# Optimization experiments

Hardware: AMD Instinct MI355X
Metric: run time of the kernel (lower is better)

The kernel has to match this reference:

```python
import jax, jax.numpy as jnp
import numpy as np

B, H = 1, 512
NVAR, NCLS = 16384, 65536
NP, NM = 4096, 4096
NEG = -1e30


def setup_inputs() -> dict:
    key = jax.random.key(0)
    ks = jax.random.split(key, 16)
    s = 0.02  # weight init scale
    return {
        "literal_emb": jax.random.normal(ks[0], (B, 2 * NVAR, H), jnp.float32),
        "clause_emb": jax.random.normal(ks[1], (B, NCLS, H), jnp.float32),
        "pos_idx": jax.random.randint(ks[2], (NP,), 0, NCLS),
        "neg_idx": jax.random.randint(ks[3], (NM,), 0, NCLS),
        "keep_mask": jax.random.randint(ks[4], (NP, NM), 0, 2).astype(bool),
        "taken_mask": jax.random.uniform(ks[5], (NP, NM)) < 0.01,  # sparse exclusion set
        "var_K_w": s * jax.random.normal(ks[6], (H, H), jnp.float32),
        "var_K_b": jnp.zeros((H,), jnp.float32),
        "var_Q_w": s * jax.random.normal(ks[7], (H, H), jnp.float32),
        "var_Q_b": jnp.zeros((H,), jnp.float32),
        "var_attn_w": s * jax.random.normal(ks[8], (1, H), jnp.float32),
        "var_attn_b": jnp.zeros((1,), jnp.float32),
        "W_Q_w": s * jax.random.normal(ks[9], (H, H), jnp.float32),
        "W_Q_b": jnp.zeros((H,), jnp.float32),
        "W_K_w": s * jax.random.normal(ks[10], (H, H), jnp.float32),
        "W_K_b": jnp.zeros((H,), jnp.float32),
    }


def reference(literal_emb, clause_emb, pos_idx, neg_idx, keep_mask, taken_mask,
              var_K_w, var_K_b, var_Q_w, var_Q_b, var_attn_w, var_attn_b,
              W_Q_w, W_Q_b, W_K_w, W_K_b):
    n_vars = literal_emb.shape[1] // 2
    # --- select_var: additive attention over positive literals ---
    K = literal_emb[:, :n_vars]                       # [B, V, H]
    K_t = K @ var_K_w.T + var_K_b                     # [B, V, H]
    Q = clause_emb.sum(axis=1)                        # [B, H] (C_aggr='sum')
    Q_t = Q @ var_Q_w.T + var_Q_b                     # [B, H]
    u = (jnp.tanh(K_t + Q_t[:, None, :]) @ var_attn_w.T + var_attn_b)[..., 0]  # [B, V]
    log_score = jax.nn.log_softmax(u, axis=-1)
    var_logp = jnp.max(log_score, axis=-1)            # [B]
    var_idx = jnp.argmax(log_score, axis=-1)          # [B]
    # --- clause-pair attention over pivot pos/neg clause pools ---
    q = clause_emb[:, pos_idx] @ W_Q_w.T + W_Q_b      # [B, NP, H]
    k = clause_emb[:, neg_idx] @ W_K_w.T + W_K_b      # [B, NM, H]
    h = q.shape[-1]
    scores = jnp.einsum('bnh,bmh->bnm', q, k) / jnp.sqrt(jnp.float32(h))
    # mask_grid_asym: drop invalid (keep_mask==0) and already-taken pairs, log-normalize
    valid = keep_mask & (~taken_mask)                 # [NP, NM]
    masked = jnp.where(valid[None], scores, jnp.float32(NEG))
    flat = masked.reshape(masked.shape[0], -1)        # [B, NP*NM]
    logp = jax.nn.log_softmax(flat, axis=-1)
    C_logp = jnp.max(logp, axis=-1)                   # [B]
    C_flat = jnp.argmax(logp, axis=-1)                # [B]
    M = scores.shape[-1]
    ci, cj = C_flat // M, C_flat % M
    c_idx_pos = pos_idx[ci]                           # map back to global clause ids
    c_idx_neg = neg_idx[cj]
    c_logp = C_logp + var_logp                        # [B]
    return (c_logp, c_idx_pos, c_idx_neg, var_idx)
```

## Files before the change

kernel.cpp:

```cpp
#include <hip/hip_runtime.h>
#include <hip/hip_bf16.h>
#include <math.h>

#define HH 512
#define NVARS 16384
#define NPOS 4096
#define NMS 4096
#define NEGV -1.0e30f
#define RSQRT_H 0.04419417382415922f

#define BM 128
#define BK 16

typedef unsigned short u16;
typedef __attribute__((ext_vector_type(8))) short bf16x8;
typedef __attribute__((ext_vector_type(4))) float f32x4;

struct SPart { float m; float s; int a; int pad; };

__device__ inline u16 f2bf(float f) {
  unsigned u = __float_as_uint(f);
  unsigned r = (u + 0x7fffu + ((u >> 16) & 1u)) >> 16;
  return (u16)r;
}
__device__ inline float bf2f(u16 h) { return __uint_as_float(((unsigned)h) << 16); }

__device__ inline void wreduce_maxidx(float& v, int& idx) {
#pragma unroll
  for (int m = 1; m < 64; m <<= 1) {
    float ov = __shfl_xor(v, m, 64);
    int oi = __shfl_xor(idx, m, 64);
    if (ov > v || (ov == v && oi < idx)) { v = ov; idx = oi; }
  }
}

__device__ inline float wreduce_sum(float v) {
#pragma unroll
  for (int m = 1; m < 64; m <<= 1) v += __shfl_xor(v, m, 64);
  return v;
}

__global__ void detect_kernel(const unsigned int* __restrict__ keep, int* __restrict__ flag) {
  if (threadIdx.x == 0 && blockIdx.x == 0) {
    int ok = 1;
    for (int i = 0; i < 64; ++i) if (keep[i] > 1u) ok = 0;
    *flag = ok;
  }
}

__global__ __launch_bounds__(256) void pack_kernel(
    const void* __restrict__ keep, const void* __restrict__ taken,
    const int* __restrict__ flag, unsigned long long* __restrict__ vmask) {
  __shared__ unsigned char nib[256];
  const int f = *flag;
  const int t = threadIdx.x;
  const size_t e = (size_t)blockIdx.x * 1024 + (size_t)t * 4;
  int v0, v1, v2, v3;
  if (f) {
    uint4 kv = *(const uint4*)((const unsigned int*)keep + e);
    uint4 tv = *(const uint4*)((const unsigned int*)taken + e);
    v0 = kv.x && !tv.x; v1 = kv.y && !tv.y; v2 = kv.z && !tv.z; v3 = kv.w && !tv.w;
  } else {
    unsigned kv = *(const unsigned*)((const unsigned char*)keep + e);
    unsigned tv = *(const unsigned*)((const unsigned char*)taken + e);
    v0 = (kv & 0xffu) && !(tv & 0xffu);
    v1 = (kv & 0xff00u) && !(tv & 0xff00u);
    v2 = (kv & 0xff0000u) && !(tv & 0xff0000u);
    v3 = (kv & 0xff000000u) && !(tv & 0xff000000u);
  }
  nib[t] = (unsigned char)(v0 | (v1 << 1) | (v2 << 2) | (v3 << 3));
  __syncthreads();
  if (t < 16) {
    unsigned long long m = 0;
#pragma unroll
    for (int j = 0; j < 16; ++j)
      m |= (unsigned long long)nib[t * 16 + j] << (4 * j);
    vmask[(size_t)blockIdx.x * 16 + t] = m;
  }
}

__global__ __launch_bounds__(256) void qsum_kernel(
    const float* __restrict__ clause, double* __restrict__ qpart) {
  const int b = blockIdx.x, t = threadIdx.x;
  const int fg = t & 127;
  const int rh = t >> 7;
  const float* base = clause + (size_t)(b * 128 + rh * 64) * HH + fg * 4;
  double a0 = 0.0, a1 = 0.0, a2 = 0.0, a3 = 0.0;
#pragma unroll 4
  for (int r = 0; r < 64; ++r) {
    float4 v = *(const float4*)(base + (size_t)r * HH);
    a0 += (double)v.x; a1 += (double)v.y; a2 += (double)v.z; a3 += (double)v.w;
  }
  double* o = qpart + (size_t)(b * 2 + rh) * HH + fg * 4;
  o[0] = a0; o[1] = a1; o[2] = a2; o[3] = a3;
}

__global__ __launch_bounds__(256) void qred_kernel(
    const double* __restrict__ qpart, double* __restrict__ Qd) {
  __shared__ double red[256];
  const int t = threadIdx.x;
  const int h = blockIdx.x * 16 + (t & 15);
  const int chunk = t >> 4;
  double s = 0.0;
  for (int j = 0; j < 64; ++j) s += qpart[(size_t)(chunk * 64 + j) * HH + h];
  red[t] = s;
  __syncthreads();
  for (int off = 8; off > 0; off >>= 1) {
    if (chunk < off) red[t] += red[t + off * 16];
    __syncthreads();
  }
  if (t < 16) Qd[blockIdx.x * 16 + t] = red[t];
}

__global__ __launch_bounds__(256) void prepmv_kernel(
    const double* __restrict__ Qd, const float* __restrict__ varQw,
    const float* __restrict__ varQb, const float* __restrict__ varKb,
    float* __restrict__ tvec) {
  __shared__ double red[256];
  const int t = threadIdx.x;
  const int h = blockIdx.x * 16 + (t & 15);
  const int chunk = t >> 4;
  const float* wrow = varQw + (size_t)h * HH + chunk * 32;
  const double* qd = Qd + chunk * 32;
  double s = 0.0;
  for (int j = 0; j < 32; ++j) s += qd[j] * (double)wrow[j];
  red[t] = s;
  __syncthreads();
  for (int off = 8; off > 0; off >>= 1) {
    if (chunk < off) red[t] += red[t + off * 16];
    __syncthreads();
  }
  if (t < 16) {
    int hh = blockIdx.x * 16 + t;
    tvec[hh] = (float)(red[t] + (double)varQb[hh] + (double)varKb[hh]);
  }
}

__global__ __launch_bounds__(256) void tofrag_kernel(
    const float* __restrict__ src, u16* __restrict__ hi, u16* __restrict__ lo) {
  const int frag = blockIdx.x * 4 + (threadIdx.x >> 6);
  const int lane = threadIdx.x & 63;
  const int R = frag >> 4, K = frag & 15;
  const float* p = src + (size_t)(R * 16 + (lane & 15)) * HH + K * 32 + (lane >> 4) * 8;
  float v[8];
  *(float4*)&v[0] = *(const float4*)p;
  *(float4*)&v[4] = *(const float4*)(p + 4);
  u16 h[8], l[8];
#pragma unroll
  for (int e = 0; e < 8; ++e) { h[e] = f2bf(v[e]); l[e] = f2bf(v[e] - bf2f(h[e])); }
  size_t base = (size_t)frag * 512 + (size_t)lane * 8;
  *(ushort4*)(hi + base) = *(ushort4*)&h[0];
  *(ushort4*)(hi + base + 4) = *(ushort4*)&h[4];
  *(ushort4*)(lo + base) = *(ushort4*)&l[0];
  *(ushort4*)(lo + base + 4) = *(ushort4*)&l[4];
}

#define MFMA16(A, B)                                                                 \
  _Pragma("unroll") for (int i_ = 0; i_ < 4; ++i_)                                   \
  _Pragma("unroll") for (int j_ = 0; j_ < 4; ++j_)                                   \
    acc[i_][j_] = __builtin_amdgcn_mfma_f32_16x16x32_bf16(A[i_], B[j_], acc[i_][j_], 0, 0, 0);

#define MFMAS(AH, AL, BH, BL)                                                        \
  do { MFMA16(AH, BH) MFMA16(AH, BL) MFMA16(AL, BH) } while (0)

#define LOADF(s, AH, AL, BH, BL, PAH, PAL, PBH, PBL)                                 \
  do {                                                                               \
    _Pragma("unroll") for (int f_ = 0; f_ < 4; ++f_) {                               \
      size_t oa_ = abase + (size_t)f_ * 8192 + (size_t)(s) * 512;                    \
      size_t ob_ = bbase + (size_t)f_ * 8192 + (size_t)(s) * 512;                    \
      AH[f_] = *(const bf16x8*)(PAH + oa_);                                          \
      AL[f_] = *(const bf16x8*)(PAL + oa_);                                          \
      BH[f_] = *(const bf16x8*)(PBH + ob_);                                          \
      BL[f_] = *(const bf16x8*)(PBL + ob_);                                          \
    }                                                                                \
  } while (0)

__global__ __launch_bounds__(256, 3) void proj_kernel(
    const float* __restrict__ clause,
    const int* __restrict__ pos_idx, const int* __restrict__ neg_idx,
    const u16* __restrict__ wqhi, const u16* __restrict__ wqlo,
    const u16* __restrict__ wkhi2, const u16* __restrict__ wklo2,
    const float* __restrict__ bQ, const float* __restrict__ bK,
    float* __restrict__ qmat, float* __restrict__ kmat) {
  const int* __restrict__ idx = blockIdx.z ? neg_idx : pos_idx;
  const u16* __restrict__ bhp = blockIdx.z ? wkhi2 : wqhi;
  const u16* __restrict__ blp = blockIdx.z ? wklo2 : wqlo;
  const float* __restrict__ bias = blockIdx.z ? bK : bQ;
  float* __restrict__ out = blockIdx.z ? kmat : qmat;

  const int t = threadIdx.x, lane = t & 63, wid = t >> 6;
  const int wn = wid & 1, wm = wid >> 1;
  const int row0 = blockIdx.x * 128;
  const int col0 = blockIdx.y * 128;

  const float* aptr[4];
#pragma unroll
  for (int f = 0; f < 4; ++f) {
    int g = idx[row0 + wn * 64 + f * 16 + (lane & 15)];
    aptr[f] = clause + (size_t)g * HH + (lane >> 4) * 8;
  }
  const size_t bbase = (size_t)((col0 >> 4) + wm * 4) * 8192 + (size_t)lane * 8;

  f32x4 acc[4][4] = {};
#pragma unroll
  for (int s = 0; s < 16; ++s) {
    float rA[4][8];
    bf16x8 aH[4], aL[4], bH[4], bL[4];
#pragma unroll
    for (int f = 0; f < 4; ++f) {
      *(float4*)&rA[f][0] = *(const float4*)(aptr[f] + s * 32);
      *(float4*)&rA[f][4] = *(const float4*)(aptr[f] + s * 32 + 4);
      size_t ob = bbase + (size_t)f * 8192 + (size_t)s * 512;
      bH[f] = *(const bf16x8*)(bhp + ob);
      bL[f] = *(const bf16x8*)(blp + ob);
    }
#pragma unroll
    for (int f = 0; f < 4; ++f)
#pragma unroll
      for (int e = 0; e < 8; ++e) {
        float v = rA[f][e];
        u16 h = f2bf(v);
        aH[f][e] = (short)h;
        aL[f][e] = (short)f2bf(v - bf2f(h));
      }
    MFMAS(aH, aL, bH, bL);
  }

#pragma unroll
  for (int i = 0; i < 4; ++i)
#pragma unroll
    for (int j = 0; j < 4; ++j) {
      int h = col0 + wm * 64 + j * 16 + (lane & 15);
      float b = bias[h];
#pragma unroll
      for (int r = 0; r < 4; ++r) {
        int n = row0 + wn * 64 + i * 16 + (lane >> 4) * 4 + r;
        out[(size_t)n * HH + h] = acc[i][j][r] + b;
      }
    }
}

__global__ __launch_bounds__(256, 3) void ktu_kernel(
    const u16* __restrict__ lithi, const u16* __restrict__ litlo,
    const u16* __restrict__ wkhi, const u16* __restrict__ wklo,
    const float* __restrict__ tvec, const float* __restrict__ attnw,
    float* __restrict__ upart) {
  const int t = threadIdx.x, lane = t & 63, wid = t >> 6;
  const int wn = wid & 1, wm = wid >> 1;
  const int row0 = blockIdx.x * 128;
  const size_t abase = (size_t)((row0 >> 4) + wn * 4) * 8192 + (size_t)lane * 8;
  const size_t bbase = (size_t)(blockIdx.y * 8 + wm * 4) * 8192 + (size_t)lane * 8;

  f32x4 acc[4][4] = {};
#pragma unroll
  for (int s = 0; s < 16; ++s) {
    bf16x8 aH[4], aL[4], bH[4], bL[4];
    LOADF(s, aH, aL, bH, bL, lithi, litlo, wkhi, wklo);
    MFMAS(aH, aL, bH, bL);
  }

  const int cbase = blockIdx.y * 128 + wm * 64;
  float tv[4], aw[4];
#pragma unroll
  for (int j = 0; j < 4; ++j) {
    int c = cbase + j * 16 + (lane & 15);
    tv[j] = tvec[c]; aw[j] = attnw[c];
  }
  float us[4][4];
#pragma unroll
  for (int i = 0; i < 4; ++i)
#pragma unroll
    for (int r = 0; r < 4; ++r) {
      float s = 0.f;
#pragma unroll
      for (int j = 0; j < 4; ++j) {
        float x = acc[i][j][r] + tv[j];
        float th = 1.0f - 2.0f / (__expf(2.0f * x) + 1.0f);
        s += th * aw[j];
      }
      us[i][r] = s;
    }
#pragma unroll
  for (int m = 1; m < 16; m <<= 1)
#pragma unroll
    for (int i = 0; i < 4; ++i)
#pragma unroll
      for (int r = 0; r < 4; ++r) us[i][r] += __shfl_xor(us[i][r], m, 64);
  if ((lane & 15) == 0) {
#pragma unroll
    for (int i = 0; i < 4; ++i)
#pragma unroll
      for (int r = 0; r < 4; ++r) {
        int row = row0 + wn * 64 + i * 16 + (lane >> 4) * 4 + r;
        upart[(size_t)(blockIdx.y * 2 + wm) * NVARS + row] = us[i][r];
      }
  }
}

__global__ __launch_bounds__(256, 3) void scores_kernel(
    const u16* __restrict__ qhi, const u16* __restrict__ qlo,
    const u16* __restrict__ khi, const u16* __restrict__ klo,
    const unsigned long long* __restrict__ vmask, SPart* __restrict__ parts) {
  __shared__ unsigned long long mrow[128][2];
  __shared__ float s_rv[4]; __shared__ int s_ri[4]; __shared__ float s_rs[4];
  __shared__ float s_bm; __shared__ int s_ba;

  const int t = threadIdx.x;
  const int lane = t & 63;
  const int wid = t >> 6;
  const int wn = wid & 1, wm = wid >> 1;

  const int bid = blockIdx.x;
  const int xcd = bid & 7, p = bid >> 3;
  const int sp = p >> 6, q = p & 63;
  const int g = xcd * 2 + sp;
  const int bx = (g & 3) * 8 + (q & 7);
  const int by = (g >> 2) * 8 + (q >> 3);

  const int n0 = by * 128;
  const int m0 = bx * 128;
  const size_t abase = (size_t)((n0 >> 4) + wn * 4) * 8192 + (size_t)lane * 8;
  const size_t bbase = (size_t)((m0 >> 4) + wm * 4) * 8192 + (size_t)lane * 8;

  {
    int r = t >> 1, w = t & 1;
    mrow[r][w] = vmask[(size_t)(n0 + r) * (NMS / 64) + (m0 >> 6) + w];
  }
  __syncthreads();

  f32x4 acc[4][4] = {};
#pragma unroll
  for (int s = 0; s < 16; ++s) {
    bf16x8 aH[4], aL[4], bH[4], bL[4];
    LOADF(s, aH, aL, bH, bL, qhi, qlo, khi, klo);
    MFMAS(aH, aL, bH, bL);
  }

  const int rbase = wn * 64 + (lane >> 4) * 4;
  const int cb15 = (lane & 15);

  float mv = NEGV; int mi = 0x7fffffff;
#pragma unroll
  for (int i = 0; i < 4; ++i) {
#pragma unroll
    for (int r = 0; r < 4; ++r) {
      int rl = rbase + i * 16 + r;
      unsigned long long ww = mrow[rl][wm];
      int gb = (n0 + rl) * NMS + m0;
#pragma unroll
      for (int j = 0; j < 4; ++j) {
        int bit = j * 16 + cb15;
        int cl = wm * 64 + bit;
        float sv = acc[i][j][r] * RSQRT_H;
        acc[i][j][r] = sv;
        bool valid = ((ww >> bit) & 1ull) != 0;
        if (valid && (sv > mv || (sv == mv && gb + cl < mi))) { mv = sv; mi = gb + cl; }
      }
    }
  }
  wreduce_maxidx(mv, mi);
  if ((t & 63) == 0) { s_rv[wid] = mv; s_ri[wid] = mi; }
  __syncthreads();
  if (t == 0) {
    float bm = s_rv[0]; int ba = s_ri[0];
    for (int w = 1; w < 4; ++w)
      if (s_rv[w] > bm || (s_rv[w] == bm && s_ri[w] < ba)) { bm = s_rv[w]; ba = s_ri[w]; }
    s_bm = bm; s_ba = ba;
  }
  __syncthreads();
  const float bm = s_bm;

  float se = 0.f;
#pragma unroll
  for (int i = 0; i < 4; ++i) {
#pragma unroll
    for (int r = 0; r < 4; ++r) {
      int rl = rbase + i * 16 + r;
      unsigned long long ww = mrow[rl][wm];
#pragma unroll
      for (int j = 0; j < 4; ++j) {
        int bit = j * 16 + cb15;
        bool valid = ((ww >> bit) & 1ull) != 0;
        if (valid) se += __expf(acc[i][j][r] - bm);
      }
    }
  }
  se = wreduce_sum(se);
  if ((t & 63) == 0) s_rs[wid] = se;
  __syncthreads();
  if (t == 0) {
    SPart pt;
    pt.m = s_bm;
    pt.s = s_rs[0] + s_rs[1] + s_rs[2] + s_rs[3];
    pt.a = s_ba; pt.pad = 0;
    parts[by * 32 + bx] = pt;
  }
}

__global__ __launch_bounds__(256) void usum_kernel(
    const float* __restrict__ upart, SPart* __restrict__ uparts2) {
  __shared__ float s_rv[4]; __shared__ int s_ri[4]; __shared__ float s_rs[4];
  __shared__ float s_bm; __shared__ int s_ba;
  const int t = threadIdx.x;
  const int i = blockIdx.x * 256 + t;
  float u = 0.f;
#pragma unroll
  for (int p = 0; p < 8; ++p) u += upart[(size_t)p * NVARS + i];
  float mv = u; int mi = i;
  wreduce_maxidx(mv, mi);
  if ((t & 63) == 0) { s_rv[t >> 6] = mv; s_ri[t >> 6] = mi; }
  __syncthreads();
  if (t == 0) {
    float bm = s_rv[0]; int ba = s_ri[0];
    for (int w = 1; w < 4; ++w)
      if (s_rv[w] > bm || (s_rv[w] == bm && s_ri[w] < ba)) { bm = s_rv[w]; ba = s_ri[w]; }
    s_bm = bm; s_ba = ba;
  }
  __syncthreads();
  float se = __expf(u - s_bm);
  se = wreduce_sum(se);
  if ((t & 63) == 0) s_rs[t >> 6] = se;
  __syncthreads();
  if (t == 0) {
    SPart p;
    p.m = s_bm;
    p.s = s_rs[0] + s_rs[1] + s_rs[2] + s_rs[3];
    p.a = s_ba; p.pad = 0;
    uparts2[blockIdx.x] = p;
  }
}

__global__ __launch_bounds__(256) void final_kernel(
    const SPart* __restrict__ uparts2, const SPart* __restrict__ parts,
    const int* __restrict__ pos_idx, const int* __restrict__ neg_idx,
    float* __restrict__ out) {
  __shared__ float s_rv[4]; __shared__ int s_ri[4]; __shared__ float s_rs[4];
  __shared__ float s_umax; __shared__ int s_uarg; __shared__ float s_usum;
  __shared__ float s_gm; __shared__ int s_ga;
  const int t = threadIdx.x;

  float mv = -3.0e38f; int mi = 0x7fffffff;
  SPart up;
  if (t < 64) {
    up = uparts2[t];
    mv = up.m; mi = up.a;
  }
  wreduce_maxidx(mv, mi);
  if ((t & 63) == 0) { s_rv[t >> 6] = mv; s_ri[t >> 6] = mi; }
  __syncthreads();
  if (t == 0) {
    float bm = s_rv[0]; int ba = s_ri[0];
    for (int w = 1; w < 4; ++w)
      if (s_rv[w] > bm || (s_rv[w] == bm && s_ri[w] < ba)) { bm = s_rv[w]; ba = s_ri[w]; }
    s_umax = bm; s_uarg = ba;
  }
  __syncthreads();
  float se = (t < 64) ? up.s * __expf(up.m - s_umax) : 0.f;
  se = wreduce_sum(se);
  if ((t & 63) == 0) s_rs[t >> 6] = se;
  __syncthreads();
  if (t == 0) s_usum = s_rs[0] + s_rs[1] + s_rs[2] + s_rs[3];
  __syncthreads();

  mv = NEGV; mi = 0x7fffffff;
  for (int i = t; i < 1024; i += 256) {
    SPart p = parts[i];
    if (p.m > mv || (p.m == mv && p.a < mi)) { mv = p.m; mi = p.a; }
  }
  wreduce_maxidx(mv, mi);
  if ((t & 63) == 0) { s_rv[t >> 6] = mv; s_ri[t >> 6] = mi; }
  __syncthreads();
  if (t == 0) {
    float bm = s_rv[0]; int ba = s_ri[0];
    for (int w = 1; w < 4; ++w)
      if (s_rv[w] > bm || (s_rv[w] == bm && s_ri[w] < ba)) { bm = s_rv[w]; ba = s_ri[w]; }
    s_gm = bm; s_ga = ba;
  }
  __syncthreads();
  const float gm = s_gm;
  float ss = 0.f;
  for (int i = t; i < 1024; i += 256) {
    SPart p = parts[i];
    ss += p.s * __expf(p.m - gm);
  }
  ss = wreduce_sum(ss);
  if ((t & 63) == 0) s_rs[t >> 6] = ss;
  __syncthreads();
  if (t == 0) {
    float gsum = s_rs[0] + s_rs[1] + s_rs[2] + s_rs[3];
    float c_logp = -logf(gsum) - logf(s_usum);
    int ga = s_ga;
    if (ga == 0x7fffffff) ga = 0;
    int ci = ga >> 12, cj = ga & 4095;
    out[0] = c_logp;
    out[1] = (float)pos_idx[ci];
    out[2] = (float)neg_idx[cj];
    out[3] = (float)s_uarg;
  }
}

extern "C" void kernel_launch(void* const* d_in, const int* in_sizes, int n_in,
                              void* d_out, int out_size, void* d_ws, size_t ws_size,
                              hipStream_t stream) {
  (void)in_sizes; (void)n_in; (void)out_size; (void)ws_size;
  const float* lit    = (const float*)d_in[0];
  const float* clause = (const float*)d_in[1];
  const int* pos_idx  = (const int*)d_in[2];
  const int* neg_idx  = (const int*)d_in[3];
  const void* keep    = d_in[4];
  const void* taken   = d_in[5];
  const float* varKw  = (const float*)d_in[6];
  const float* varKb  = (const float*)d_in[7];
  const float* varQw  = (const float*)d_in[8];
  const float* varQb  = (const float*)d_in[9];
  const float* attnw  = (const float*)d_in[10];
  const float* WQw    = (const float*)d_in[12];
  const float* WQb    = (const float*)d_in[13];
  const float* WKw    = (const float*)d_in[14];
  const float* WKb    = (const float*)d_in[15];

  char* ws = (char*)d_ws;
  size_t off = 0;
  auto alloc = [&](size_t b) {
    char* p = ws + off;
    off = (off + b + 255) & ~(size_t)255;
    return p;
  };
  int* flag                  = (int*)alloc(4);
  double* qpart              = (double*)alloc((size_t)1024 * HH * 8);
  double* Qd                 = (double*)alloc(HH * 8);
  float* tvec                = (float*)alloc(HH * 4);
  float* upart               = (float*)alloc(8 * (size_t)NVARS * 4);
  unsigned long long* vmask  = (unsigned long long*)alloc((size_t)NPOS * (NMS / 64) * 8);
  float* qmat                = (float*)alloc((size_t)NPOS * HH * 4);
  float* kmat                = (float*)alloc((size_t)NMS * HH * 4);
  u16* qhi                   = (u16*)alloc((size_t)NPOS * HH * 2);
  u16* qlo                   = (u16*)alloc((size_t)NPOS * HH * 2);
  u16* khi                   = (u16*)alloc((size_t)NMS * HH * 2);
  u16* klo                   = (u16*)alloc((size_t)NMS * HH * 2);
  u16* wkhi                  = (u16*)alloc((size_t)HH * HH * 2);
  u16* wklo                  = (u16*)alloc((size_t)HH * HH * 2);
  u16* pwqhi                 = (u16*)alloc((size_t)HH * HH * 2);
  u16* pwqlo                 = (u16*)alloc((size_t)HH * HH * 2);
  u16* pwkhi                 = (u16*)alloc((size_t)HH * HH * 2);
  u16* pwklo                 = (u16*)alloc((size_t)HH * HH * 2);
  u16* lithi                 = (u16*)alloc((size_t)NVARS * HH * 2);
  u16* litlo                 = (u16*)alloc((size_t)NVARS * HH * 2);
  SPart* parts               = (SPart*)alloc(1024 * sizeof(SPart));
  SPart* uparts2             = (SPart*)alloc(64 * sizeof(SPart));

  detect_kernel<<<1, 64, 0, stream>>>((const unsigned int*)keep, flag);
  pack_kernel<<<16384, 256, 0, stream>>>(keep, taken, flag, vmask);
  qsum_kernel<<<512, 256, 0, stream>>>(clause, qpart);
  qred_kernel<<<32, 256, 0, stream>>>(qpart, Qd);
  prepmv_kernel<<<32, 256, 0, stream>>>(Qd, varQw, varQb, varKb, tvec);
  tofrag_kernel<<<128, 256, 0, stream>>>(varKw, wkhi, wklo);
  tofrag_kernel<<<128, 256, 0, stream>>>(WQw, pwqhi, pwqlo);
  tofrag_kernel<<<128, 256, 0, stream>>>(WKw, pwkhi, pwklo);
  tofrag_kernel<<<4096, 256, 0, stream>>>(lit, lithi, litlo);
  proj_kernel<<<dim3(32, 4, 2), 256, 0, stream>>>(clause, pos_idx, neg_idx,
                                                  pwqhi, pwqlo, pwkhi, pwklo,
                                                  WQb, WKb, qmat, kmat);
  tofrag_kernel<<<1024, 256, 0, stream>>>(qmat, qhi, qlo);
  tofrag_kernel<<<1024, 256, 0, stream>>>(kmat, khi, klo);
  ktu_kernel<<<dim3(128, 4), 256, 0, stream>>>(lithi, litlo, wkhi, wklo,
                                               tvec, attnw, upart);
  scores_kernel<<<1024, 256, 0, stream>>>(qhi, qlo, khi, klo, vmask, parts);
  usum_kernel<<<64, 256, 0, stream>>>(upart, uparts2);
  final_kernel<<<1, 256, 0, stream>>>(uparts2, parts, pos_idx, neg_idx,
                                      (float*)d_out);
}
```

Measured before the change: 262.0 us.

## Stage MFMA fragments through double-buffered LDS with direct global-to-LDS loads

The ktu and scores GEMM kernels now cooperatively stage the hi/lo bf16 fragments into a double-buffered shared-memory tile using global_load_lds. Each wave fetches one operand stream, so the fragments shared across waves are read from global memory once per block. The next k-slice's load is issued before the current slice's MFMAs to overlap memory and compute. Separately, the detect_kernel launch is removed and each pack block checks the mask format inline. The cost is 64 KB of LDS per block, a lower occupancy hint (2 instead of 3), and a barrier per k-step.

After: 222.0 us. 1.18x faster.

```diff
diff --git a/kernel.cpp b/kernel.cpp
--- a/kernel.cpp
+++ b/kernel.cpp
@@ -40,19 +40,20 @@
   return v;
 }
 
-__global__ void detect_kernel(const unsigned int* __restrict__ keep, int* __restrict__ flag) {
-  if (threadIdx.x == 0 && blockIdx.x == 0) {
-    int ok = 1;
-    for (int i = 0; i < 64; ++i) if (keep[i] > 1u) ok = 0;
-    *flag = ok;
-  }
+__device__ __forceinline__ void stage_frag(const u16* src, u16* dst) {
+  __builtin_amdgcn_global_load_lds(
+      (const __attribute__((address_space(1))) void*)src,
+      (__attribute__((address_space(3))) void*)dst, 16, 0, 0);
 }
 
 __global__ __launch_bounds__(256) void pack_kernel(
     const void* __restrict__ keep, const void* __restrict__ taken,
-    const int* __restrict__ flag, unsigned long long* __restrict__ vmask) {
+    unsigned long long* __restrict__ vmask) {
   __shared__ unsigned char nib[256];
-  const int f = *flag;
+  const unsigned* kw = (const unsigned*)keep;
+  int f = 1;
+#pragma unroll
+  for (int i = 0; i < 16; ++i) f &= (kw[i] <= 1u);
   const int t = threadIdx.x;
   const size_t e = (size_t)blockIdx.x * 1024 + (size_t)t * 4;
   int v0, v1, v2, v3;
@@ -163,18 +164,6 @@
 #define MFMAS(AH, AL, BH, BL)                                                        \
   do { MFMA16(AH, BH) MFMA16(AH, BL) MFMA16(AL, BH) } while (0)
 
-#define LOADF(s, AH, AL, BH, BL, PAH, PAL, PBH, PBL)                                 \
-  do {                                                                               \
-    _Pragma("unroll") for (int f_ = 0; f_ < 4; ++f_) {                               \
-      size_t oa_ = abase + (size_t)f_ * 8192 + (size_t)(s) * 512;                    \
-      size_t ob_ = bbase + (size_t)f_ * 8192 + (size_t)(s) * 512;                    \
-      AH[f_] = *(const bf16x8*)(PAH + oa_);                                          \
-      AL[f_] = *(const bf16x8*)(PAL + oa_);                                          \
-      BH[f_] = *(const bf16x8*)(PBH + ob_);                                          \
-      BL[f_] = *(const bf16x8*)(PBL + ob_);                                          \
-    }                                                                                \
-  } while (0)
-
 __global__ __launch_bounds__(256, 3) void proj_kernel(
     const float* __restrict__ clause,
     const int* __restrict__ pos_idx, const int* __restrict__ neg_idx,
@@ -240,24 +229,45 @@
     }
 }
 
-__global__ __launch_bounds__(256, 3) void ktu_kernel(
+
+__global__ __launch_bounds__(256, 2) void ktu_kernel(
     const u16* __restrict__ lithi, const u16* __restrict__ litlo,
     const u16* __restrict__ wkhi, const u16* __restrict__ wklo,
     const float* __restrict__ tvec, const float* __restrict__ attnw,
     float* __restrict__ upart) {
+  __shared__ __align__(16) u16 lds[2][4][8][512];
   const int t = threadIdx.x, lane = t & 63, wid = t >> 6;
   const int wn = wid & 1, wm = wid >> 1;
   const int row0 = blockIdx.x * 128;
-  const size_t abase = (size_t)((row0 >> 4) + wn * 4) * 8192 + (size_t)lane * 8;
-  const size_t bbase = (size_t)(blockIdx.y * 8 + wm * 4) * 8192 + (size_t)lane * 8;
-
+  const int l8 = lane * 8;
+
+  const u16* sa = (wid == 0) ? lithi : (wid == 1) ? litlo : (wid == 2) ? wkhi : wklo;
+  const int rb = (wid < 2) ? (row0 >> 4) : (blockIdx.y * 8);
+  const u16* sab = sa + (size_t)rb * 8192 + l8;
+
+#define KSTAGE(buf, s)                                                        \
+  _Pragma("unroll") for (int f_ = 0; f_ < 8; ++f_)                            \
+    stage_frag(sab + (size_t)f_ * 8192 + (size_t)(s) * 512,                   \
+               &lds[buf][wid][f_][0]);
+
+  KSTAGE(0, 0)
   f32x4 acc[4][4] = {};
 #pragma unroll
   for (int s = 0; s < 16; ++s) {
+    __syncthreads();
+    if (s < 15) { KSTAGE((s + 1) & 1, s + 1) }
+    const int b = s & 1;
     bf16x8 aH[4], aL[4], bH[4], bL[4];
-    LOADF(s, aH, aL, bH, bL, lithi, litlo, wkhi, wklo);
+#pragma unroll
+    for (int f = 0; f < 4; ++f) {
+      aH[f] = *(const bf16x8*)&lds[b][0][wn * 4 + f][l8];
+      aL[f] = *(const bf16x8*)&lds[b][1][wn * 4 + f][l8];
+      bH[f] = *(const bf16x8*)&lds[b][2][wm * 4 + f][l8];
+      bL[f] = *(const bf16x8*)&lds[b][3][wm * 4 + f][l8];
+    }
     MFMAS(aH, aL, bH, bL);
   }
+#undef KSTAGE
 
   const int cbase = blockIdx.y * 128 + wm * 64;
   float tv[4], aw[4];
@@ -297,10 +307,11 @@
   }
 }
 
-__global__ __launch_bounds__(256, 3) void scores_kernel(
+__global__ __launch_bounds__(256, 2) void scores_kernel(
     const u16* __restrict__ qhi, const u16* __restrict__ qlo,
     const u16* __restrict__ khi, const u16* __restrict__ klo,
     const unsigned long long* __restrict__ vmask, SPart* __restrict__ parts) {
+  __shared__ __align__(16) u16 lds[2][4][8][512];
   __shared__ unsigned long long mrow[128][2];
   __shared__ float s_rv[4]; __shared__ int s_ri[4]; __shared__ float s_rs[4];
   __shared__ float s_bm; __shared__ int s_ba;
@@ -309,6 +320,7 @@
   const int lane = t & 63;
   const int wid = t >> 6;
   const int wn = wid & 1, wm = wid >> 1;
+  const int l8 = lane * 8;
 
   const int bid = blockIdx.x;
   const int xcd = bid & 7, p = bid >> 3;
@@ -319,22 +331,39 @@
 
   const int n0 = by * 128;
   const int m0 = bx * 128;
-  const size_t abase = (size_t)((n0 >> 4) + wn * 4) * 8192 + (size_t)lane * 8;
-  const size_t bbase = (size_t)((m0 >> 4) + wm * 4) * 8192 + (size_t)lane * 8;
+
+  const u16* sa = (wid == 0) ? qhi : (wid == 1) ? qlo : (wid == 2) ? khi : klo;
+  const int rb = (wid < 2) ? (n0 >> 4) : (m0 >> 4);
+  const u16* sab = sa + (size_t)rb * 8192 + l8;
+
+#define SSTAGE(buf, s)                                                        \
+  _Pragma("unroll") for (int f_ = 0; f_ < 8; ++f_)                            \
+    stage_frag(sab + (size_t)f_ * 8192 + (size_t)(s) * 512,                   \
+               &lds[buf][wid][f_][0]);
 
   {
     int r = t >> 1, w = t & 1;
     mrow[r][w] = vmask[(size_t)(n0 + r) * (NMS / 64) + (m0 >> 6) + w];
   }
-  __syncthreads();
-
+
+  SSTAGE(0, 0)
   f32x4 acc[4][4] = {};
 #pragma unroll
   for (int s = 0; s < 16; ++s) {
+    __syncthreads();
+    if (s < 15) { SSTAGE((s + 1) & 1, s + 1) }
+    const int b = s & 1;
     bf16x8 aH[4], aL[4], bH[4], bL[4];
-    LOADF(s, aH, aL, bH, bL, qhi, qlo, khi, klo);
+#pragma unroll
+    for (int f = 0; f < 4; ++f) {
+      aH[f] = *(const bf16x8*)&lds[b][0][wn * 4 + f][l8];
+      aL[f] = *(const bf16x8*)&lds[b][1][wn * 4 + f][l8];
+      bH[f] = *(const bf16x8*)&lds[b][2][wm * 4 + f][l8];
+      bL[f] = *(const bf16x8*)&lds[b][3][wm * 4 + f][l8];
+    }
     MFMAS(aH, aL, bH, bL);
   }
+#undef SSTAGE
 
   const int rbase = wn * 64 + (lane >> 4) * 4;
   const int cb15 = (lane & 15);
@@ -526,7 +555,6 @@
     off = (off + b + 255) & ~(size_t)255;
     return p;
   };
-  int* flag                  = (int*)alloc(4);
   double* qpart              = (double*)alloc((size_t)1024 * HH * 8);
   double* Qd                 = (double*)alloc(HH * 8);
   float* tvec                = (float*)alloc(HH * 4);
@@ -549,8 +577,7 @@
   SPart* parts               = (SPart*)alloc(1024 * sizeof(SPart));
   SPart* uparts2             = (SPart*)alloc(64 * sizeof(SPart));
 
-  detect_kernel<<<1, 64, 0, stream>>>((const unsigned int*)keep, flag);
-  pack_kernel<<<16384, 256, 0, stream>>>(keep, taken, flag, vmask);
+  pack_kernel<<<16384, 256, 0, stream>>>(keep, taken, vmask);
   qsum_kernel<<<512, 256, 0, stream>>>(clause, qpart);
   qred_kernel<<<32, 256, 0, stream>>>(qpart, Qd);
   prepmv_kernel<<<32, 256, 0, stream>>>(Qd, varQw, varQb, varKb, tvec);
```
